# Kernel optimization log

Hardware: AMD Instinct MI355X
Metric: run time of the kernel (lower is better)

## Reference

```python
import jax, jax.numpy as jnp
import numpy as np

R, B, F, H, C = 32, 2048, 512, 1024, 100  # n_rules, batch, n_fea, 2*n_fea, n_cls


def setup_inputs() -> dict:
    key = jax.random.key(0)
    ks = jax.random.split(key, 10)
    sc = lambda k, shape, fan: (jax.random.normal(k, shape, jnp.float32) / np.float32(np.sqrt(fan)))
    return {
        "data": jax.random.normal(ks[0], (B, F), jnp.float32),
        "proto": jax.random.normal(ks[1], (R, F), jnp.float32),
        "var": jax.random.uniform(ks[2], (R, F), jnp.float32, 0.5, 1.5),
        "fs_w1": sc(ks[3], (F, H), F), "fs_b1": jnp.zeros((H,), jnp.float32),
        "fs_w2": sc(ks[4], (H, F), H), "fs_b2": jnp.zeros((F,), jnp.float32),
        "fs_w3": sc(ks[5], (F, 1), F), "fs_b3": jnp.zeros((1,), jnp.float32),
        "cq_w1": sc(ks[6], (R, F, H), F), "cq_b1": jnp.zeros((R, H), jnp.float32),
        "cq_w2": sc(ks[7], (R, H, F), H), "cq_b2": jnp.zeros((R, F), jnp.float32),
        "cq_w3": sc(ks[8], (R, F, C), F), "cq_b3": jnp.zeros((R, C), jnp.float32),
        "is_train": 1,
    }


def reference(data, proto, var, fs_w1, fs_b1, fs_w2, fs_b2, fs_w3, fs_b3,
              cq_w1, cq_b1, cq_w2, cq_b2, cq_w3, cq_b3, is_train):
    # Gaussian fuzzy membership per rule: [R, B, F]
    fuzzy = jnp.exp(-(data[None, :, :] - proto[:, None, :]) ** 2
                    / (2.0 * var[:, None, :] ** 2))
    # shared fire-strength MLP applied per rule
    h = jax.nn.relu(jnp.einsum('rbf,fh->rbh', fuzzy, fs_w1) + fs_b1)
    h = jax.nn.relu(jnp.einsum('rbh,hf->rbf', h, fs_w2) + fs_b2)
    fs_logits = (jnp.einsum('rbf,fo->rbo', h, fs_w3) + fs_b3)[..., 0]  # [R, B]
    fire = jax.nn.softmax(fs_logits.T, axis=1)  # [B, R], softmax over rules
    # per-rule consequent MLPs on raw data (grouped GEMMs)
    g = jax.nn.relu(jnp.einsum('bf,rfh->rbh', data, cq_w1) + cq_b1[:, None, :])
    g = jax.nn.relu(jnp.einsum('rbh,rhf->rbf', g, cq_w2) + cq_b2[:, None, :])
    logits = jnp.einsum('rbf,rfc->rbc', g, cq_w3) + cq_b3[:, None, :]  # [R, B, C]
    # softmax-weighted expert sum, then class softmax
    out = jnp.einsum('br,rbc->bc', fire, logits)  # [B, C]
    return jax.nn.softmax(out, axis=1)
```

## Files before the change

### kernel.cpp

```cpp
#include <hip/hip_runtime.h>

typedef __attribute__((ext_vector_type(8))) short short8;
typedef __attribute__((ext_vector_type(4))) float f32x4;

__device__ __forceinline__ unsigned short f2bf(float f) {
    union { float f; unsigned u; } v; v.f = f;
    unsigned r = v.u + 0x7FFFu + ((v.u >> 16) & 1u);
    return (unsigned short)(r >> 16);
}

__global__ __launch_bounds__(256)
void cvt_bf16_kernel(const float* __restrict__ X, unsigned short* __restrict__ Y, int n4) {
    int i = blockIdx.x * 256 + threadIdx.x;
    if (i >= n4) return;
    float4 v = ((const float4*)X)[i];
    ushort4 o; o.x = f2bf(v.x); o.y = f2bf(v.y); o.z = f2bf(v.z); o.w = f2bf(v.w);
    ((ushort4*)Y)[i] = o;
}

__global__ __launch_bounds__(256)
void transpose_kernel(const float* __restrict__ X, unsigned short* __restrict__ Y,
                      int K, int N, int Np) {
    __shared__ float tile[32][33];
    int g = blockIdx.z;
    const float* Xg = X + (long)g * K * N;
    unsigned short* Yg = Y + (long)g * Np * K;
    int k0 = blockIdx.x * 32, n0 = blockIdx.y * 32;
    int tx = threadIdx.x & 31, ty = threadIdx.x >> 5;
#pragma unroll
    for (int i = 0; i < 4; ++i) {
        int kk = ty + i * 8;
        int n = n0 + tx;
        tile[kk][tx] = (n < N) ? Xg[(long)(k0 + kk) * N + n] : 0.0f;
    }
    __syncthreads();
#pragma unroll
    for (int i = 0; i < 4; ++i) {
        int nn = ty + i * 8;
        Yg[(long)(n0 + nn) * K + k0 + tx] = f2bf(tile[tx][nn]);
    }
}

__global__ __launch_bounds__(128)
void fuzzy_kernel(const float* __restrict__ data, const float* __restrict__ proto,
                  const float* __restrict__ var, unsigned short* __restrict__ fuzzy) {
    int rb = blockIdx.x;
    int r = rb >> 11, b = rb & 2047;
    int f = threadIdx.x * 4;
    float4 d = *(const float4*)(data + (long)b * 512 + f);
    float4 p = *(const float4*)(proto + (long)r * 512 + f);
    float4 w = *(const float4*)(var + (long)r * 512 + f);
    ushort4 o;
    float x;
    x = d.x - p.x; o.x = f2bf(__expf(-(x * x) / (2.f * w.x * w.x)));
    x = d.y - p.y; o.y = f2bf(__expf(-(x * x) / (2.f * w.y * w.y)));
    x = d.z - p.z; o.z = f2bf(__expf(-(x * x) / (2.f * w.z * w.z)));
    x = d.w - p.w; o.w = f2bf(__expf(-(x * x) / (2.f * w.w * w.w)));
    *(ushort4*)(fuzzy + (long)rb * 512 + f) = o;
}

template<int EPI, bool RELU>
__global__ __launch_bounds__(256, 2)
void gemm128_kernel(const unsigned short* __restrict__ A,
                    const unsigned short* __restrict__ Bt,
                    const float* __restrict__ bias,
                    void* __restrict__ Cptr,
                    const float* __restrict__ w3,
                    float* __restrict__ fsl_or_mix,
                    const float* __restrict__ fire,
                    int nM, int nN, int K,
                    long sAg, long sBg, long sCg, int sBiasG, int biasN, int r0) {
    unsigned tot = gridDim.x, bid = blockIdx.x;
    unsigned sw = (bid & 7u) * (tot >> 3) + (bid >> 3);
    unsigned pg = (unsigned)nM * (unsigned)nN;
    unsigned g = sw / pg;
    unsigned rem = sw - g * pg;
    const int m0 = (int)(rem / (unsigned)nN) * 128;
    const int n0 = (int)(rem % (unsigned)nN) * 128;
    const int N = nN * 128;
    A += (long)g * sAg; Bt += (long)g * sBg; bias += (long)g * sBiasG;

    __shared__ __align__(16) unsigned short ldsA[128 * 32];
    __shared__ __align__(16) unsigned short ldsB[128 * 32];

    const int tid = threadIdx.x;
    const int lane = tid & 63;
    const int w = tid >> 6;
    const int wm = w >> 1, wn = w & 1;
    const int r16 = lane & 15, kg = lane >> 4;

    f32x4 acc[4][4];
#pragma unroll
    for (int i = 0; i < 4; ++i)
#pragma unroll
        for (int j = 0; j < 4; ++j) {
            f32x4 z = {0.f, 0.f, 0.f, 0.f};
            acc[i][j] = z;
        }

    for (int k0 = 0; k0 < K; k0 += 32) {
#pragma unroll
        for (int j = 0; j < 2; ++j) {
            int t = j * 256 + tid;
            int row = t >> 2, sl = t & 3;
            int kc = (sl ^ ((row >> 1) & 3)) << 3;
            const unsigned short* ga = A + (long)(m0 + row) * K + k0 + kc;
            __builtin_amdgcn_global_load_lds(
                (const __attribute__((address_space(1))) void*)ga,
                (__attribute__((address_space(3))) void*)(ldsA + (j * 256 + tid) * 8),
                16, 0, 0);
            const unsigned short* gb = Bt + (long)(n0 + row) * K + k0 + kc;
            __builtin_amdgcn_global_load_lds(
                (const __attribute__((address_space(1))) void*)gb,
                (__attribute__((address_space(3))) void*)(ldsB + (j * 256 + tid) * 8),
                16, 0, 0);
        }
        __syncthreads();
        short8 aF[4], bF[4];
#pragma unroll
        for (int mt = 0; mt < 4; ++mt) {
            int R = wm * 64 + mt * 16 + r16;
            aF[mt] = *(const short8*)(ldsA + R * 32 + ((kg ^ ((R >> 1) & 3)) << 3));
        }
#pragma unroll
        for (int nt = 0; nt < 4; ++nt) {
            int R = wn * 64 + nt * 16 + r16;
            bF[nt] = *(const short8*)(ldsB + R * 32 + ((kg ^ ((R >> 1) & 3)) << 3));
        }
#pragma unroll
        for (int mt = 0; mt < 4; ++mt)
#pragma unroll
            for (int nt = 0; nt < 4; ++nt)
                acc[mt][nt] = __builtin_amdgcn_mfma_f32_16x16x32_bf16(
                    aF[mt], bF[nt], acc[mt][nt], 0, 0, 0);
        __syncthreads();
    }

    if constexpr (EPI == 1) {
        float w3v[4], bv[4];
#pragma unroll
        for (int nt = 0; nt < 4; ++nt) {
            int col = n0 + wn * 64 + nt * 16 + r16;
            w3v[nt] = w3[col];
            bv[nt] = bias[col];
        }
#pragma unroll
        for (int mt = 0; mt < 4; ++mt) {
#pragma unroll
            for (int j = 0; j < 4; ++j) {
                float p = 0.f;
#pragma unroll
                for (int nt = 0; nt < 4; ++nt) {
                    float v = acc[mt][nt][j] + bv[nt];
                    if (RELU) v = fmaxf(v, 0.f);
                    p += v * w3v[nt];
                }
                p += __shfl_xor(p, 1, 64);
                p += __shfl_xor(p, 2, 64);
                p += __shfl_xor(p, 4, 64);
                p += __shfl_xor(p, 8, 64);
                if (r16 == 0) {
                    int row = m0 + wm * 64 + mt * 16 + kg * 4 + j;
                    atomicAdd(&fsl_or_mix[row], p);
                }
            }
        }
    } else if constexpr (EPI == 3) {
        float bv[4];
#pragma unroll
        for (int nt = 0; nt < 4; ++nt) {
            int col = n0 + wn * 64 + nt * 16 + r16;
            bv[nt] = (col < biasN) ? bias[col] : 0.f;
        }
#pragma unroll
        for (int mt = 0; mt < 4; ++mt) {
#pragma unroll
            for (int j = 0; j < 4; ++j) {
                int row = m0 + wm * 64 + mt * 16 + kg * 4 + j;
                float f = fire[row * 32 + r0 + (int)g];
#pragma unroll
                for (int nt = 0; nt < 4; ++nt) {
                    int col = n0 + wn * 64 + nt * 16 + r16;
                    atomicAdd(&fsl_or_mix[row * 128 + col], f * (acc[mt][nt][j] + bv[nt]));
                }
            }
        }
    } else {
        __shared__ __align__(16) unsigned short ldsC[128 * 136];
        float bv[4];
#pragma unroll
        for (int nt = 0; nt < 4; ++nt) {
            int col = n0 + wn * 64 + nt * 16 + r16;
            bv[nt] = (col < biasN) ? bias[col] : 0.f;
        }
#pragma unroll
        for (int mt = 0; mt < 4; ++mt) {
            int rl = wm * 64 + mt * 16 + kg * 4;
#pragma unroll
            for (int nt = 0; nt < 4; ++nt) {
                int cc = wn * 64 + nt * 16 + r16;
#pragma unroll
                for (int j = 0; j < 4; ++j) {
                    float v = acc[mt][nt][j] + bv[nt];
                    if (RELU) v = fmaxf(v, 0.f);
                    ldsC[(rl + j) * 136 + cc] = f2bf(v);
                }
            }
        }
        __syncthreads();
        unsigned short* Cg = (unsigned short*)Cptr + (long)g * sCg;
#pragma unroll
        for (int rnd = 0; rnd < 8; ++rnd) {
            int idx = rnd * 256 + tid;
            int row = idx >> 4, c8 = idx & 15;
            short8 vv = *(const short8*)(ldsC + row * 136 + c8 * 8);
            *(short8*)(Cg + (long)(m0 + row) * N + n0 + c8 * 8) = vv;
        }
    }
}

__global__ __launch_bounds__(256)
void fire_kernel(const float* __restrict__ fslog, float* __restrict__ fire) {
    int b = blockIdx.x * 256 + threadIdx.x;
    float v[32];
    float mx = -1e30f;
#pragma unroll
    for (int r = 0; r < 32; ++r) { v[r] = fslog[r * 2048 + b]; mx = fmaxf(mx, v[r]); }
    float s = 0.f;
#pragma unroll
    for (int r = 0; r < 32; ++r) { v[r] = __expf(v[r] - mx); s += v[r]; }
    float inv = 1.f / s;
#pragma unroll
    for (int r = 0; r < 32; ++r) fire[b * 32 + r] = v[r] * inv;
}

__global__ __launch_bounds__(128)
void softmax_out_kernel(const float* __restrict__ mix, float* __restrict__ out) {
    int b = blockIdx.x, c = threadIdx.x;
    __shared__ float redm[2], reds[2];
    float val = (c < 100) ? mix[b * 128 + c] : -1e30f;
    float m = val;
#pragma unroll
    for (int off = 32; off; off >>= 1) m = fmaxf(m, __shfl_xor(m, off, 64));
    int lane = c & 63, wv = c >> 6;
    if (lane == 0) redm[wv] = m;
    __syncthreads();
    m = fmaxf(redm[0], redm[1]);
    float e = (c < 100) ? __expf(val - m) : 0.f;
    float s = e;
#pragma unroll
    for (int off = 32; off; off >>= 1) s += __shfl_xor(s, off, 64);
    if (lane == 0) reds[wv] = s;
    __syncthreads();
    s = reds[0] + reds[1];
    if (c < 100) out[b * 100 + c] = e / s;
}

extern "C" void kernel_launch(void* const* d_in, const int* in_sizes, int n_in,
                              void* d_out, int out_size, void* d_ws, size_t ws_size,
                              hipStream_t stream) {
    const float* data  = (const float*)d_in[0];
    const float* proto = (const float*)d_in[1];
    const float* var   = (const float*)d_in[2];
    const float* fs_w1 = (const float*)d_in[3];
    const float* fs_b1 = (const float*)d_in[4];
    const float* fs_w2 = (const float*)d_in[5];
    const float* fs_b2 = (const float*)d_in[6];
    const float* fs_w3 = (const float*)d_in[7];
    const float* cq_w1 = (const float*)d_in[9];
    const float* cq_b1 = (const float*)d_in[10];
    const float* cq_w2 = (const float*)d_in[11];
    const float* cq_b2 = (const float*)d_in[12];
    const float* cq_w3 = (const float*)d_in[13];
    const float* cq_b3 = (const float*)d_in[14];
    float* out = (float*)d_out;

    const size_t PERSIST = 2097152 + 1048576 + 1048576 + 262144 + 262144 + 1048576;
    const size_t H1SZ = (size_t)65536 * 1024 * 2;
    const size_t FUZZSZ = (size_t)65536 * 512 * 2;
    auto need = [&](int p) -> size_t {
        size_t fz = FUZZSZ > (size_t)p * 2097152 ? FUZZSZ : (size_t)p * 2097152;
        return PERSIST + H1SZ + fz + (size_t)p * (1048576 + 1048576 + 131072);
    };
    int p2r = 16;
    while (need(p2r) > ws_size && p2r > 2) p2r >>= 1;

    char* ws = (char*)d_ws;
    size_t off = 0;
    auto take = [&](size_t bytes) { char* p = ws + off; off += bytes; return p; };
    unsigned short* data_bf = (unsigned short*)take(2097152);
    unsigned short* w1t     = (unsigned short*)take(1048576);
    unsigned short* w2t     = (unsigned short*)take(1048576);
    float*          fslog   = (float*)take(262144);
    float*          fire    = (float*)take(262144);
    float*          mix     = (float*)take(1048576);
    unsigned short* h1      = (unsigned short*)take(H1SZ);
    size_t fzsz = FUZZSZ > (size_t)p2r * 2097152 ? FUZZSZ : (size_t)p2r * 2097152;
    unsigned short* fuzzy   = (unsigned short*)take(fzsz);
    unsigned short* cW1t    = (unsigned short*)take((size_t)p2r * 1048576);
    unsigned short* cW2t    = (unsigned short*)take((size_t)p2r * 1048576);
    unsigned short* cW3t    = (unsigned short*)take((size_t)p2r * 131072);
    unsigned short* g1 = h1;
    unsigned short* g2 = fuzzy;

    cvt_bf16_kernel<<<1024, 256, 0, stream>>>(data, data_bf, 262144);
    transpose_kernel<<<dim3(16, 32, 1), 256, 0, stream>>>(fs_w1, w1t, 512, 1024, 1024);
    transpose_kernel<<<dim3(32, 16, 1), 256, 0, stream>>>(fs_w2, w2t, 1024, 512, 512);
    hipMemsetAsync(fslog, 0, 262144, stream);
    hipMemsetAsync(mix, 0, 1048576, stream);

    fuzzy_kernel<<<65536, 128, 0, stream>>>(data, proto, var, fuzzy);
    gemm128_kernel<0, true><<<512 * 8, 256, 0, stream>>>(
        fuzzy, w1t, fs_b1, h1, nullptr, nullptr, nullptr,
        512, 8, 512, 0, 0, 0, 0, 1024, 0);
    gemm128_kernel<1, true><<<512 * 4, 256, 0, stream>>>(
        h1, w2t, fs_b2, nullptr, fs_w3, fslog, nullptr,
        512, 4, 1024, 0, 0, 0, 0, 512, 0);
    fire_kernel<<<8, 256, 0, stream>>>(fslog, fire);

    for (int ch = 0; ch < 32 / p2r; ++ch) {
        const int r0 = ch * p2r;
        transpose_kernel<<<dim3(16, 32, p2r), 256, 0, stream>>>(
            cq_w1 + (long)r0 * 512 * 1024, cW1t, 512, 1024, 1024);
        transpose_kernel<<<dim3(32, 16, p2r), 256, 0, stream>>>(
            cq_w2 + (long)r0 * 1024 * 512, cW2t, 1024, 512, 512);
        transpose_kernel<<<dim3(16, 4, p2r), 256, 0, stream>>>(
            cq_w3 + (long)r0 * 512 * 100, cW3t, 512, 100, 128);
        gemm128_kernel<0, true><<<16 * 8 * p2r, 256, 0, stream>>>(
            data_bf, cW1t, cq_b1 + (long)r0 * 1024, g1, nullptr, nullptr, nullptr,
            16, 8, 512, 0, (long)1024 * 512, (long)2048 * 1024, 1024, 1024, 0);
        gemm128_kernel<0, true><<<16 * 4 * p2r, 256, 0, stream>>>(
            g1, cW2t, cq_b2 + (long)r0 * 512, g2, nullptr, nullptr, nullptr,
            16, 4, 1024, (long)2048 * 1024, (long)512 * 1024, (long)2048 * 512, 512, 512, 0);
        gemm128_kernel<3, false><<<16 * 1 * p2r, 256, 0, stream>>>(
            g2, cW3t, cq_b3 + (long)r0 * 100, nullptr, nullptr, mix, fire,
            16, 1, 512, (long)2048 * 512, (long)128 * 512, 0, 100, 100, r0);
    }
    softmax_out_kernel<<<2048, 128, 0, stream>>>(mix, out);
}
```

Baseline: 571.6 us.

## Fuse data bf16 conversion into fuzzy kernel and hoist consequent weight transposes

Removes the separate data-to-bf16 kernel by writing data_bf from the fuzzy kernel for rule 0, and makes the fuzzy kernel handle two rows per 256-thread block. All 32 consequent weight transposes are hoisted out of the chunk loop into three large launches, with the transposed weights stored in now-dead regions of the h1 and fuzzy buffers, so the workspace-size fallback is dropped and 16 rules per chunk is fixed. The GEMM LDS is unified into one 32KB buffer shared by the A/B tiles and the epilogue staging, removing the padded 136-stride C tile; this may add LDS bank conflicts but lowers LDS use and could help occupancy. Aliasing the weight copies into h1/fuzzy relies on those buffers being dead after the fire-strength stage.

```diff
diff --git a/kernel.cpp b/kernel.cpp
--- a/kernel.cpp
+++ b/kernel.cpp
@@ -7,15 +7,6 @@
     union { float f; unsigned u; } v; v.f = f;
     unsigned r = v.u + 0x7FFFu + ((v.u >> 16) & 1u);
     return (unsigned short)(r >> 16);
-}
-
-__global__ __launch_bounds__(256)
-void cvt_bf16_kernel(const float* __restrict__ X, unsigned short* __restrict__ Y, int n4) {
-    int i = blockIdx.x * 256 + threadIdx.x;
-    if (i >= n4) return;
-    float4 v = ((const float4*)X)[i];
-    ushort4 o; o.x = f2bf(v.x); o.y = f2bf(v.y); o.z = f2bf(v.z); o.w = f2bf(v.w);
-    ((ushort4*)Y)[i] = o;
 }
 
 __global__ __launch_bounds__(256)
@@ -41,12 +32,14 @@
     }
 }
 
-__global__ __launch_bounds__(128)
+__global__ __launch_bounds__(256)
 void fuzzy_kernel(const float* __restrict__ data, const float* __restrict__ proto,
-                  const float* __restrict__ var, unsigned short* __restrict__ fuzzy) {
-    int rb = blockIdx.x;
+                  const float* __restrict__ var, unsigned short* __restrict__ fuzzy,
+                  unsigned short* __restrict__ data_bf) {
+    int t = threadIdx.x;
+    int rb = blockIdx.x * 2 + (t >> 7);
     int r = rb >> 11, b = rb & 2047;
-    int f = threadIdx.x * 4;
+    int f = (t & 127) * 4;
     float4 d = *(const float4*)(data + (long)b * 512 + f);
     float4 p = *(const float4*)(proto + (long)r * 512 + f);
     float4 w = *(const float4*)(var + (long)r * 512 + f);
@@ -57,6 +50,11 @@
     x = d.z - p.z; o.z = f2bf(__expf(-(x * x) / (2.f * w.z * w.z)));
     x = d.w - p.w; o.w = f2bf(__expf(-(x * x) / (2.f * w.w * w.w)));
     *(ushort4*)(fuzzy + (long)rb * 512 + f) = o;
+    if (r == 0) {
+        ushort4 od;
+        od.x = f2bf(d.x); od.y = f2bf(d.y); od.z = f2bf(d.z); od.w = f2bf(d.w);
+        *(ushort4*)(data_bf + (long)b * 512 + f) = od;
+    }
 }
 
 template<int EPI, bool RELU>
@@ -71,7 +69,7 @@
                     int nM, int nN, int K,
                     long sAg, long sBg, long sCg, int sBiasG, int biasN, int r0) {
     unsigned tot = gridDim.x, bid = blockIdx.x;
-    unsigned sw = (bid & 7u) * (tot >> 3) + (bid >> 3);
+    unsigned sw = (tot & 7u) == 0 ? (bid & 7u) * (tot >> 3) + (bid >> 3) : bid;
     unsigned pg = (unsigned)nM * (unsigned)nN;
     unsigned g = sw / pg;
     unsigned rem = sw - g * pg;
@@ -80,8 +78,9 @@
     const int N = nN * 128;
     A += (long)g * sAg; Bt += (long)g * sBg; bias += (long)g * sBiasG;
 
-    __shared__ __align__(16) unsigned short ldsA[128 * 32];
-    __shared__ __align__(16) unsigned short ldsB[128 * 32];
+    __shared__ __align__(16) unsigned short ldsU[128 * 128];
+    unsigned short* ldsA = ldsU;
+    unsigned short* ldsB = ldsU + 4096;
 
     const int tid = threadIdx.x;
     const int lane = tid & 63;
@@ -186,7 +185,6 @@
             }
         }
     } else {
-        __shared__ __align__(16) unsigned short ldsC[128 * 136];
         float bv[4];
 #pragma unroll
         for (int nt = 0; nt < 4; ++nt) {
@@ -203,7 +201,7 @@
                 for (int j = 0; j < 4; ++j) {
                     float v = acc[mt][nt][j] + bv[nt];
                     if (RELU) v = fmaxf(v, 0.f);
-                    ldsC[(rl + j) * 136 + cc] = f2bf(v);
+                    ldsU[(rl + j) * 128 + cc] = f2bf(v);
                 }
             }
         }
@@ -213,7 +211,7 @@
         for (int rnd = 0; rnd < 8; ++rnd) {
             int idx = rnd * 256 + tid;
             int row = idx >> 4, c8 = idx & 15;
-            short8 vv = *(const short8*)(ldsC + row * 136 + c8 * 8);
+            short8 vv = *(const short8*)(ldsU + row * 128 + c8 * 8);
             *(short8*)(Cg + (long)(m0 + row) * N + n0 + c8 * 8) = vv;
         }
     }
@@ -275,16 +273,8 @@
     const float* cq_b3 = (const float*)d_in[14];
     float* out = (float*)d_out;
 
-    const size_t PERSIST = 2097152 + 1048576 + 1048576 + 262144 + 262144 + 1048576;
-    const size_t H1SZ = (size_t)65536 * 1024 * 2;
+    const size_t H1SZ   = (size_t)65536 * 1024 * 2;
     const size_t FUZZSZ = (size_t)65536 * 512 * 2;
-    auto need = [&](int p) -> size_t {
-        size_t fz = FUZZSZ > (size_t)p * 2097152 ? FUZZSZ : (size_t)p * 2097152;
-        return PERSIST + H1SZ + fz + (size_t)p * (1048576 + 1048576 + 131072);
-    };
-    int p2r = 16;
-    while (need(p2r) > ws_size && p2r > 2) p2r >>= 1;
-
     char* ws = (char*)d_ws;
     size_t off = 0;
     auto take = [&](size_t bytes) { char* p = ws + off; off += bytes; return p; };
@@ -295,21 +285,20 @@
     float*          fire    = (float*)take(262144);
     float*          mix     = (float*)take(1048576);
     unsigned short* h1      = (unsigned short*)take(H1SZ);
-    size_t fzsz = FUZZSZ > (size_t)p2r * 2097152 ? FUZZSZ : (size_t)p2r * 2097152;
-    unsigned short* fuzzy   = (unsigned short*)take(fzsz);
-    unsigned short* cW1t    = (unsigned short*)take((size_t)p2r * 1048576);
-    unsigned short* cW2t    = (unsigned short*)take((size_t)p2r * 1048576);
-    unsigned short* cW3t    = (unsigned short*)take((size_t)p2r * 131072);
-    unsigned short* g1 = h1;
-    unsigned short* g2 = fuzzy;
-
-    cvt_bf16_kernel<<<1024, 256, 0, stream>>>(data, data_bf, 262144);
+    unsigned short* fuzzy   = (unsigned short*)take(FUZZSZ);
+    unsigned short* g1   = h1;
+    unsigned short* cW1t = h1 + (size_t)33554432;
+    unsigned short* cW2t = h1 + (size_t)50331648;
+    unsigned short* g2   = fuzzy;
+    unsigned short* cW3t = fuzzy + (size_t)16777216;
+    const int p2r = 16;
+
     transpose_kernel<<<dim3(16, 32, 1), 256, 0, stream>>>(fs_w1, w1t, 512, 1024, 1024);
     transpose_kernel<<<dim3(32, 16, 1), 256, 0, stream>>>(fs_w2, w2t, 1024, 512, 512);
     hipMemsetAsync(fslog, 0, 262144, stream);
     hipMemsetAsync(mix, 0, 1048576, stream);
 
-    fuzzy_kernel<<<65536, 128, 0, stream>>>(data, proto, var, fuzzy);
+    fuzzy_kernel<<<32768, 256, 0, stream>>>(data, proto, var, fuzzy, data_bf);
     gemm128_kernel<0, true><<<512 * 8, 256, 0, stream>>>(
         fuzzy, w1t, fs_b1, h1, nullptr, nullptr, nullptr,
         512, 8, 512, 0, 0, 0, 0, 1024, 0);
@@ -318,22 +307,23 @@
         512, 4, 1024, 0, 0, 0, 0, 512, 0);
     fire_kernel<<<8, 256, 0, stream>>>(fslog, fire);
 
+    transpose_kernel<<<dim3(16, 32, 32), 256, 0, stream>>>(cq_w1, cW1t, 512, 1024, 1024);
+    transpose_kernel<<<dim3(32, 16, 32), 256, 0, stream>>>(cq_w2, cW2t, 1024, 512, 512);
+    transpose_kernel<<<dim3(16, 4, 32), 256, 0, stream>>>(cq_w3, cW3t, 512, 100, 128);
+
     for (int ch = 0; ch < 32 / p2r; ++ch) {
         const int r0 = ch * p2r;
-        transpose_kernel<<<dim3(16, 32, p2r), 256, 0, stream>>>(
-            cq_w1 + (long)r0 * 512 * 1024, cW1t, 512, 1024, 1024);
-        transpose_kernel<<<dim3(32, 16, p2r), 256, 0, stream>>>(
-            cq_w2 + (long)r0 * 1024 * 512, cW2t, 1024, 512, 512);
-        transpose_kernel<<<dim3(16, 4, p2r), 256, 0, stream>>>(
-            cq_w3 + (long)r0 * 512 * 100, cW3t, 512, 100, 128);
         gemm128_kernel<0, true><<<16 * 8 * p2r, 256, 0, stream>>>(
-            data_bf, cW1t, cq_b1 + (long)r0 * 1024, g1, nullptr, nullptr, nullptr,
+            data_bf, cW1t + (long)r0 * 1024 * 512, cq_b1 + (long)r0 * 1024, g1,
+            nullptr, nullptr, nullptr,
             16, 8, 512, 0, (long)1024 * 512, (long)2048 * 1024, 1024, 1024, 0);
         gemm128_kernel<0, true><<<16 * 4 * p2r, 256, 0, stream>>>(
-            g1, cW2t, cq_b2 + (long)r0 * 512, g2, nullptr, nullptr, nullptr,
+            g1, cW2t + (long)r0 * 512 * 1024, cq_b2 + (long)r0 * 512, g2,
+            nullptr, nullptr, nullptr,
             16, 4, 1024, (long)2048 * 1024, (long)512 * 1024, (long)2048 * 512, 512, 512, 0);
         gemm128_kernel<3, false><<<16 * 1 * p2r, 256, 0, stream>>>(
-            g2, cW3t, cq_b3 + (long)r0 * 100, nullptr, nullptr, mix, fire,
+            g2, cW3t + (long)r0 * 128 * 512, cq_b3 + (long)r0 * 100, nullptr,
+            nullptr, mix, fire,
             16, 1, 512, (long)2048 * 512, (long)128 * 512, 0, 100, 100, r0);
     }
     softmax_out_kernel<<<2048, 128, 0, stream>>>(mix, out);
```

After: 525.1 us. 8.1% less time.
